# Optimization experiments

Measured on AMD Instinct MI355X. Metric: run time of the kernel, lower is better.

Reference implementation:

```python
import jax, jax.numpy as jnp
import numpy as np

B, D_IN, H1, H2, OUT = 8, 1024, 2048, 1024, 5120

def setup_inputs() -> dict:
    key = jax.random.key(0)
    ks = jax.random.split(key, 5)
    s1 = (6.0 / (D_IN + H1)) ** 0.5  # xavier_uniform-like scale
    s2 = (6.0 / (H1 + H2)) ** 0.5
    s3 = (6.0 / (H2 + OUT)) ** 0.5
    return {
        "x": jax.random.normal(ks[0], (B, D_IN), dtype=jnp.float32),
        "W1": jax.random.uniform(ks[1], (D_IN, H1), jnp.float32, -s1, s1),
        "b1": jnp.zeros((H1,), jnp.float32),
        "W2": jax.random.uniform(ks[2], (H1, H2), jnp.float32, -s2, s2),
        "b2": jnp.zeros((H2,), jnp.float32),
        "W3": jax.random.uniform(ks[3], (H2, OUT), jnp.float32, -s3, s3),
        "b3": jnp.zeros((OUT,), jnp.float32),
        "CM": jax.random.uniform(ks[4], (OUT, OUT), jnp.float32),
    }

def reference(x, W1, b1, W2, b2, W3, b3, CM):
    # MLP stack (eval mode: dropout is identity)
    h = jax.nn.relu(x @ W1 + b1)
    h = jax.nn.relu(h @ W2 + b2)
    features = h
    logits = h @ W3 + b3                      # [B, OUT]
    # tropical-style correlation: max_k logits[b,k] * CM[o,k]
    out = jnp.max(logits[:, None, :] * CM[None, :, :], axis=-1)  # [B, OUT]
    return out.astype(jnp.float32), features
```

## Files before the change

### kernel.cpp

```cpp
#include <hip/hip_runtime.h>
#include <cstdint>

#define B8   8
#define DIN  1024
#define NH1  2048
#define NH2  1024
#define NOUT 5120

__device__ __forceinline__ float4 ld4(const float* p) {
  return *reinterpret_cast<const float4*>(p);
}
__device__ __forceinline__ void st4(float* p, float4 v) {
  *reinterpret_cast<float4*>(p) = v;
}

template<int K, int N, int KSPLIT, int NPART, bool RELU_IN, bool WRITE_STAGE>
__global__ __launch_bounds__(256)
void gemm8(const float* __restrict__ Asrc, const float* __restrict__ bias_in,
           const float* __restrict__ W, float* __restrict__ Cparts,
           float* __restrict__ stage_out)
{
  constexpr int KC    = K / KSPLIT;
  constexpr int KC4   = KC / 4;
  constexpr int NCOLB = N / 64;
  constexpr int KT    = KC / 16;

  __shared__ float A_lds[8][KC];
  __shared__ float red[16][8][64];

  const int tid = threadIdx.x;
  const int kb  = blockIdx.x / NCOLB;
  const int cb  = blockIdx.x % NCOLB;
  const int k0  = kb * KC;

  for (int e = tid; e < 8 * KC4; e += 256) {
    const int b = e / KC4, k4 = e - b * KC4;
    float4 v;
    if constexpr (NPART == 0) {
      v = ld4(&Asrc[(size_t)b * K + k0 + 4 * k4]);
    } else {
      v = ld4(&bias_in[k0 + 4 * k4]);
      #pragma unroll
      for (int p = 0; p < NPART; ++p) {
        float4 t = ld4(&Asrc[((size_t)p * 8 + b) * K + k0 + 4 * k4]);
        v.x += t.x; v.y += t.y; v.z += t.z; v.w += t.w;
      }
      if constexpr (RELU_IN) {
        v.x = fmaxf(v.x, 0.f); v.y = fmaxf(v.y, 0.f);
        v.z = fmaxf(v.z, 0.f); v.w = fmaxf(v.w, 0.f);
      }
    }
    st4(&A_lds[b][4 * k4], v);
    if constexpr (WRITE_STAGE) {
      if (cb == 0) st4(&stage_out[(size_t)b * K + k0 + 4 * k4], v);
    }
  }
  __syncthreads();

  const int g  = tid & 15, ks = tid >> 4;
  const int c0 = cb * 64 + g * 4;
  float4 acc[8];
  #pragma unroll
  for (int b = 0; b < 8; ++b) acc[b] = make_float4(0.f, 0.f, 0.f, 0.f);

  const float* Wp = &W[(size_t)(k0 + ks * KT) * N + c0];
  #pragma unroll
  for (int i = 0; i < KT; i += 4) {
    const float4 w0 = ld4(Wp + (size_t)(i + 0) * N);
    const float4 w1 = ld4(Wp + (size_t)(i + 1) * N);
    const float4 w2 = ld4(Wp + (size_t)(i + 2) * N);
    const float4 w3 = ld4(Wp + (size_t)(i + 3) * N);
    const int kk = ks * KT + i;
    #pragma unroll
    for (int b = 0; b < 8; ++b) {
      const float4 a = ld4(&A_lds[b][kk]);
      acc[b].x += a.x * w0.x + a.y * w1.x + a.z * w2.x + a.w * w3.x;
      acc[b].y += a.x * w0.y + a.y * w1.y + a.z * w2.y + a.w * w3.y;
      acc[b].z += a.x * w0.z + a.y * w1.z + a.z * w2.z + a.w * w3.z;
      acc[b].w += a.x * w0.w + a.y * w1.w + a.z * w2.w + a.w * w3.w;
    }
  }

  __syncthreads();
  #pragma unroll
  for (int b = 0; b < 8; ++b) st4(&red[ks][b][g * 4], acc[b]);
  __syncthreads();

  for (int p = tid; p < 512; p += 256) {
    const int c = p & 63, b = p >> 6;
    float s = 0.f;
    #pragma unroll
    for (int j = 0; j < 16; ++j) s += red[j][b][c];
    Cparts[((size_t)kb * 8 + b) * N + cb * 64 + c] = s;
  }
}

__global__ __launch_bounds__(256)
void finalize_logits(const float* __restrict__ parts, const float* __restrict__ b3,
                     float* __restrict__ logits)
{
  const int i  = blockIdx.x * 256 + threadIdx.x;
  const int b  = i / 1280, k4 = i - b * 1280;
  float4 v = ld4(&b3[4 * k4]);
  #pragma unroll
  for (int p = 0; p < 4; ++p) {
    const float4 t = ld4(&parts[((size_t)p * 8 + b) * NOUT + 4 * k4]);
    v.x += t.x; v.y += t.y; v.z += t.z; v.w += t.w;
  }
  st4(&logits[(size_t)b * NOUT + 4 * k4], v);
}

__global__ __launch_bounds__(256)
void tropical8(const float* __restrict__ logits, const float* __restrict__ CM,
               float* __restrict__ out)
{
  __shared__ float L[8][1024];

  const int tid = threadIdx.x;
  const int w   = tid >> 6;
  const int l   = tid & 63;
  const int o0  = blockIdx.x * 8 + w * 2;

  float pmax[2][8];
  #pragma unroll
  for (int r = 0; r < 2; ++r)
    #pragma unroll
    for (int b = 0; b < 8; ++b) pmax[r][b] = -3.402823466e38f;

  for (int ck = 0; ck < NOUT; ck += 1024) {
    for (int e = tid; e < 2048; e += 256) {
      const int b = e >> 8, k4 = e & 255;
      st4(&L[b][4 * k4], ld4(&logits[(size_t)b * NOUT + ck + 4 * k4]));
    }

    float4 cm[2][4];
    #pragma unroll
    for (int r = 0; r < 2; ++r) {
      const float* cmrow = &CM[(size_t)(o0 + r) * NOUT + ck + 4 * l];
      #pragma unroll
      for (int i = 0; i < 4; ++i) cm[r][i] = ld4(cmrow + 256 * i);
    }

    __syncthreads();

    #pragma unroll
    for (int i = 0; i < 4; ++i) {
      const int kk = 4 * l + 256 * i;
      #pragma unroll
      for (int b = 0; b < 8; ++b) {
        const float4 lv = ld4(&L[b][kk]);
        #pragma unroll
        for (int r = 0; r < 2; ++r) {
          const float4 C = cm[r][i];
          const float m0 = fmaxf(lv.x * C.x, lv.y * C.y);
          const float m1 = fmaxf(lv.z * C.z, lv.w * C.w);
          pmax[r][b] = fmaxf(pmax[r][b], fmaxf(m0, m1));
        }
      }
    }
    __syncthreads();
  }

  #pragma unroll
  for (int r = 0; r < 2; ++r) {
    #pragma unroll
    for (int b = 0; b < 8; ++b) {
      float v = pmax[r][b];
      for (int m = 32; m; m >>= 1) v = fmaxf(v, __shfl_xor(v, m));
      if (l == 0) out[(size_t)b * NOUT + o0 + r] = v;
    }
  }
}

extern "C" void kernel_launch(void* const* d_in, const int* in_sizes, int n_in,
                              void* d_out, int out_size, void* d_ws, size_t ws_size,
                              hipStream_t stream)
{
  const float* x  = (const float*)d_in[0];
  const float* W1 = (const float*)d_in[1];
  const float* b1 = (const float*)d_in[2];
  const float* W2 = (const float*)d_in[3];
  const float* b2 = (const float*)d_in[4];
  const float* W3 = (const float*)d_in[5];
  const float* b3 = (const float*)d_in[6];
  const float* CM = (const float*)d_in[7];

  float* out  = (float*)d_out;
  float* feat = out + B8 * NOUT;

  float* ws      = (float*)d_ws;
  float* parts1  = ws;
  float* parts2  = parts1 + 8  * 8 * NH1;
  float* parts3  = parts2 + 16 * 8 * NH2;
  float* logits  = parts3 + 4  * 8 * NOUT;

  gemm8<DIN, NH1, 8, 0, false, false><<<256, 256, 0, stream>>>(x, nullptr, W1, parts1, nullptr);
  gemm8<NH1, NH2, 16, 8, true, false><<<256, 256, 0, stream>>>(parts1, b1, W2, parts2, nullptr);
  gemm8<NH2, NOUT, 4, 16, true, true><<<320, 256, 0, stream>>>(parts2, b2, W3, parts3, feat);
  finalize_logits<<<40, 256, 0, stream>>>(parts3, b3, logits);
  tropical8<<<640, 256, 0, stream>>>(logits, CM, out);
}
```

Measured before the change: 52.40 us.

## Split tropical max over K halves with double-buffered CM row streaming

Replaces the tropical kernel with one that splits the K dimension into two halves across grid.y. Each block loads its logits half into LDS once and then streams 20 CM rows per block, five per wave, double-buffering the next row in registers. A small combine kernel takes the max of the two partial results. The goal is to reload the logits tile far less often and keep more CM loads in flight, at the cost of an extra launch, a partial-result buffer and heavy register use (20 float4 buffers).

```diff
diff --git a/kernel.cpp b/kernel.cpp
--- a/kernel.cpp
+++ b/kernel.cpp
@@ -6,6 +6,8 @@
 #define NH1  2048
 #define NH2  1024
 #define NOUT 5120
+#define KHALF 2560
+#define ROWS_PER_BLOCK 20
 
 __device__ __forceinline__ float4 ld4(const float* p) {
   return *reinterpret_cast<const float4*>(p);
@@ -111,65 +113,78 @@
 }
 
 __global__ __launch_bounds__(256)
-void tropical8(const float* __restrict__ logits, const float* __restrict__ CM,
-               float* __restrict__ out)
-{
-  __shared__ float L[8][1024];
+void tropical_stream(const float* __restrict__ logits, const float* __restrict__ CM,
+                     float* __restrict__ tpart)
+{
+  __shared__ float L[8][KHALF];
 
   const int tid = threadIdx.x;
   const int w   = tid >> 6;
   const int l   = tid & 63;
-  const int o0  = blockIdx.x * 8 + w * 2;
-
-  float pmax[2][8];
-  #pragma unroll
-  for (int r = 0; r < 2; ++r)
-    #pragma unroll
-    for (int b = 0; b < 8; ++b) pmax[r][b] = -3.402823466e38f;
-
-  for (int ck = 0; ck < NOUT; ck += 1024) {
-    for (int e = tid; e < 2048; e += 256) {
-      const int b = e >> 8, k4 = e & 255;
-      st4(&L[b][4 * k4], ld4(&logits[(size_t)b * NOUT + ck + 4 * k4]));
-    }
-
-    float4 cm[2][4];
-    #pragma unroll
-    for (int r = 0; r < 2; ++r) {
-      const float* cmrow = &CM[(size_t)(o0 + r) * NOUT + ck + 4 * l];
-      #pragma unroll
-      for (int i = 0; i < 4; ++i) cm[r][i] = ld4(cmrow + 256 * i);
-    }
-
-    __syncthreads();
-
-    #pragma unroll
-    for (int i = 0; i < 4; ++i) {
-      const int kk = 4 * l + 256 * i;
+  const int kh  = blockIdx.y;
+  const int k0  = kh * KHALF;
+
+  for (int e = tid; e < 5120; e += 256) {
+    const int b = e / 640, j = e - b * 640;
+    st4(&L[b][4 * j], ld4(&logits[(size_t)b * NOUT + k0 + 4 * j]));
+  }
+  __syncthreads();
+
+  const int orow0 = blockIdx.x * ROWS_PER_BLOCK + w * 5;
+
+  float4 A[10], Bv[10];
+  const float* row0 = &CM[(size_t)orow0 * NOUT + k0 + 4 * l];
+  #pragma unroll
+  for (int j = 0; j < 10; ++j) A[j] = ld4(row0 + 256 * j);
+
+  #pragma unroll
+  for (int i = 0; i < 5; ++i) {
+    if (i < 4) {
+      const float* rn = &CM[(size_t)(orow0 + i + 1) * NOUT + k0 + 4 * l];
+      if (i & 1) {
+        #pragma unroll
+        for (int j = 0; j < 10; ++j) A[j] = ld4(rn + 256 * j);
+      } else {
+        #pragma unroll
+        for (int j = 0; j < 10; ++j) Bv[j] = ld4(rn + 256 * j);
+      }
+    }
+
+    float pmax[8];
+    #pragma unroll
+    for (int b = 0; b < 8; ++b) pmax[b] = -3.402823466e38f;
+    #pragma unroll
+    for (int j = 0; j < 10; ++j) {
+      const float4 C = (i & 1) ? Bv[j] : A[j];
+      const int kk = 4 * (l + 64 * j);
       #pragma unroll
       for (int b = 0; b < 8; ++b) {
         const float4 lv = ld4(&L[b][kk]);
-        #pragma unroll
-        for (int r = 0; r < 2; ++r) {
-          const float4 C = cm[r][i];
-          const float m0 = fmaxf(lv.x * C.x, lv.y * C.y);
-          const float m1 = fmaxf(lv.z * C.z, lv.w * C.w);
-          pmax[r][b] = fmaxf(pmax[r][b], fmaxf(m0, m1));
-        }
-      }
-    }
-    __syncthreads();
-  }
-
-  #pragma unroll
-  for (int r = 0; r < 2; ++r) {
+        const float m0 = fmaxf(lv.x * C.x, lv.y * C.y);
+        const float m1 = fmaxf(lv.z * C.z, lv.w * C.w);
+        pmax[b] = fmaxf(pmax[b], fmaxf(m0, m1));
+      }
+    }
+
     #pragma unroll
     for (int b = 0; b < 8; ++b) {
-      float v = pmax[r][b];
+      float v = pmax[b];
       for (int m = 32; m; m >>= 1) v = fmaxf(v, __shfl_xor(v, m));
-      if (l == 0) out[(size_t)b * NOUT + o0 + r] = v;
-    }
-  }
+      if (l == 0) tpart[((size_t)kh * 8 + b) * NOUT + orow0 + i] = v;
+    }
+  }
+}
+
+__global__ __launch_bounds__(256)
+void tropical_combine(const float* __restrict__ tpart, float* __restrict__ out)
+{
+  const int i = blockIdx.x * 256 + threadIdx.x;
+  const float4 a = ld4(&tpart[4 * (size_t)i]);
+  const float4 b = ld4(&tpart[(size_t)8 * NOUT + 4 * (size_t)i]);
+  float4 v;
+  v.x = fmaxf(a.x, b.x); v.y = fmaxf(a.y, b.y);
+  v.z = fmaxf(a.z, b.z); v.w = fmaxf(a.w, b.w);
+  st4(&out[4 * (size_t)i], v);
 }
 
 extern "C" void kernel_launch(void* const* d_in, const int* in_sizes, int n_in,
@@ -193,10 +208,15 @@
   float* parts2  = parts1 + 8  * 8 * NH1;
   float* parts3  = parts2 + 16 * 8 * NH2;
   float* logits  = parts3 + 4  * 8 * NOUT;
+  float* tpart   = logits + 8 * NOUT;
 
   gemm8<DIN, NH1, 8, 0, false, false><<<256, 256, 0, stream>>>(x, nullptr, W1, parts1, nullptr);
   gemm8<NH1, NH2, 16, 8, true, false><<<256, 256, 0, stream>>>(parts1, b1, W2, parts2, nullptr);
   gemm8<NH2, NOUT, 4, 16, true, true><<<320, 256, 0, stream>>>(parts2, b2, W3, parts3, feat);
   finalize_logits<<<40, 256, 0, stream>>>(parts3, b3, logits);
-  tropical8<<<640, 256, 0, stream>>>(logits, CM, out);
-}
+  {
+    dim3 grid(256, 2);
+    tropical_stream<<<grid, 256, 0, stream>>>(logits, CM, tpart);
+  }
+  tropical_combine<<<40, 256, 0, stream>>>(tpart, out);
+}
```

Result: slower. 71.49 us (+36.4%).
